# Optimization experiments

Measured on AMD Instinct MI355X. Metric: run time of the kernel, lower is better.

The kernel has to match this reference:

```python
import jax, jax.numpy as jnp
import numpy as np

N_NODES = 100000
N_EDGES = 400000
B = 1024
D_XD = 78
SEQ = 1000
EMB = 128
HID = 300
NF = 32
OUT_DIM = 128


def setup_inputs():
    key = jax.random.key(0)
    ks = jax.random.split(key, 40)
    rn = lambda k, s, sc=0.05: jax.random.normal(k, s, dtype=jnp.float32) * sc
    inp = {}
    inp['x'] = rn(ks[0], (N_NODES, D_XD), 1.0)
    inp['edge_index'] = jax.random.randint(ks[1], (2, N_EDGES), 0, N_NODES, dtype=jnp.int32)
    inp['batch'] = jnp.sort(jax.random.randint(ks[2], (N_NODES,), 0, B, dtype=jnp.int32))
    inp['target'] = jax.random.randint(ks[3], (B, SEQ), 0, 26, dtype=jnp.int32)
    inp['embs'] = rn(ks[4], (B * 13, 133), 1.0)
    inp['W1'] = rn(ks[5], (D_XD, D_XD)); inp['b1'] = jnp.zeros((D_XD,), jnp.float32)
    inp['W2'] = rn(ks[6], (D_XD, D_XD * 2)); inp['b2'] = jnp.zeros((D_XD * 2,), jnp.float32)
    inp['W3'] = rn(ks[7], (D_XD * 2, D_XD * 4)); inp['b3'] = jnp.zeros((D_XD * 4,), jnp.float32)
    inp['fc_g1_w'] = rn(ks[8], (D_XD * 4, 1024)); inp['fc_g1_b'] = jnp.zeros((1024,), jnp.float32)
    inp['fc_g2_w'] = rn(ks[9], (1024, OUT_DIM)); inp['fc_g2_b'] = jnp.zeros((OUT_DIM,), jnp.float32)
    inp['emb_xt'] = rn(ks[10], (26, EMB), 1.0)
    inp['conv_w'] = rn(ks[11], (NF, SEQ, 8)); inp['conv_b'] = jnp.zeros((NF,), jnp.float32)
    inp['fc1xt_w'] = rn(ks[12], (NF * 121, OUT_DIM)); inp['fc1xt_b'] = jnp.zeros((OUT_DIM,), jnp.float32)
    inp['fg_lin_w'] = rn(ks[13], (133, HID)); inp['fg_lin_b'] = jnp.zeros((HID,), jnp.float32)
    inp['Wq'] = rn(ks[14], (HID, HID)); inp['Wk'] = rn(ks[15], (HID, HID)); inp['Wv'] = rn(ks[16], (HID, HID))
    inp['ln_g'] = jnp.ones((HID,), jnp.float32); inp['ln_b'] = jnp.zeros((HID,), jnp.float32)
    inp['fg_out_w'] = rn(ks[17], (HID, OUT_DIM)); inp['fg_out_b'] = jnp.zeros((OUT_DIM,), jnp.float32)
    inp['fc1_w'] = rn(ks[18], (3 * OUT_DIM, 1024)); inp['fc1_b'] = jnp.zeros((1024,), jnp.float32)
    inp['fc2_w'] = rn(ks[19], (1024, 512)); inp['fc2_b'] = jnp.zeros((512,), jnp.float32)
    inp['out_w'] = rn(ks[20], (512, 1)); inp['out_b'] = jnp.zeros((1,), jnp.float32)
    return inp


def _gcn_conv(h_in, W, b, src, dst, dis):
    # PyG GCNConv: x' = D^-1/2 (A+I) D^-1/2 (X W) + b
    h = h_in @ W
    norm = dis[src] * dis[dst]  # [E]
    agg = jax.ops.segment_sum(h[src] * norm[:, None], dst, num_segments=h.shape[0])
    agg = agg + h * (dis * dis)[:, None]  # self-loop term
    return agg + b


def _forward(x, embs, W1, b1, W2, b2, W3, b3, fc_g1_w, fc_g1_b, fc_g2_w, fc_g2_b,
             emb_xt, conv_w, conv_b, fc1xt_w, fc1xt_b, fg_lin_w, fg_lin_b,
             Wq, Wk, Wv, ln_g, ln_b, fg_out_w, fg_out_b,
             fc1_w, fc1_b, fc2_w, fc2_b, out_w, out_b,
             edge_index, batch, target):
    src, dst = edge_index[0], edge_index[1]
    deg = jax.ops.segment_sum(jnp.ones_like(dst, jnp.float32), dst, num_segments=x.shape[0]) + 1.0
    dis = jax.lax.rsqrt(deg)
    h = jax.nn.relu(_gcn_conv(x, W1, b1, src, dst, dis))
    h = jax.nn.relu(_gcn_conv(h, W2, b2, src, dst, dis))
    h = jax.nn.relu(_gcn_conv(h, W3, b3, src, dst, dis))
    g = jax.ops.segment_max(h, batch, num_segments=B)  # global max pool
    g = jnp.where(jnp.isfinite(g), g, 0.0)
    g = jax.nn.relu(g @ fc_g1_w + fc_g1_b)
    g = g @ fc_g2_w + fc_g2_b  # dropout is identity at eval
    # protein branch: embedding + Conv1d(in=1000, out=32, k=8) over embed axis
    e = emb_xt[target]  # [B, SEQ, EMB]
    c = jax.lax.conv_general_dilated(e, conv_w, (1,), 'VALID',
                                     dimension_numbers=('NCH', 'OIH', 'NCH'))
    c = c + conv_b[None, :, None]  # [B, 32, 121]
    xt = c.reshape(B, NF * 121) @ fc1xt_w + fc1xt_b
    # functional-group prompt branch (KANO-style): linear -> self-attn -> LN -> gather row i*13
    f = (embs @ fg_lin_w + fg_lin_b).reshape(B, 13, HID)
    q = f @ Wq; k = f @ Wk; v = f @ Wv
    attn = jax.nn.softmax(jnp.einsum('bqd,bkd->bqk', q, k) / jnp.sqrt(jnp.float32(HID)), axis=-1)
    f2 = f + jnp.einsum('bqk,bkd->bqd', attn, v)
    mu = f2.mean(-1, keepdims=True)
    var = f2.var(-1, keepdims=True)
    f2 = (f2 - mu) * jax.lax.rsqrt(var + 1e-5) * ln_g + ln_b
    fg = f2[:, 0, :] @ fg_out_w + fg_out_b  # row i*13 per molecule
    xc = jnp.concatenate([g, xt, fg], axis=1)  # [B, 3*OUT_DIM]
    xc = jax.nn.relu(xc @ fc1_w + fc1_b)
    xc = jax.nn.relu(xc @ fc2_w + fc2_b)
    return xc @ out_w + out_b


def reference(x, edge_index, batch, target, embs, W1, b1, W2, b2, W3, b3,
              fc_g1_w, fc_g1_b, fc_g2_w, fc_g2_b, emb_xt, conv_w, conv_b,
              fc1xt_w, fc1xt_b, fg_lin_w, fg_lin_b, Wq, Wk, Wv, ln_g, ln_b,
              fg_out_w, fg_out_b, fc1_w, fc1_b, fc2_w, fc2_b, out_w, out_b):
    return _forward(x, embs, W1, b1, W2, b2, W3, b3, fc_g1_w, fc_g1_b, fc_g2_w, fc_g2_b,
                    emb_xt, conv_w, conv_b, fc1xt_w, fc1xt_b, fg_lin_w, fg_lin_b,
                    Wq, Wk, Wv, ln_g, ln_b, fg_out_w, fg_out_b,
                    fc1_w, fc1_b, fc2_w, fc2_b, out_w, out_b,
                    edge_index, batch, target)
```

## Files before the change

### kernel.cpp

```cpp
#include <hip/hip_runtime.h>
#include <hip/hip_bf16.h>
#include <math.h>

#define NNODES 100000
#define NEDGES 400000
#define NB     1024
#define SEQ    1000
#define HID    300
#define NBLK1  ((NNODES + 255) / 256)

typedef __attribute__((ext_vector_type(8))) short short8;
typedef __attribute__((ext_vector_type(4))) float f32x4;

__device__ __forceinline__ float bf_lo(unsigned int v) { return __uint_as_float(v << 16); }
__device__ __forceinline__ float bf_hi(unsigned int v) { return __uint_as_float(v & 0xffff0000u); }
__device__ __forceinline__ unsigned int bf_pack(float lo, float hi) {
    __hip_bfloat16 a = __float2bfloat16(lo), b = __float2bfloat16(hi);
    unsigned short ua = *(unsigned short*)&a, ub = *(unsigned short*)&b;
    return (unsigned int)ua | ((unsigned int)ub << 16);
}

__global__ void cvt_pad_kernel(const float* __restrict__ in, __hip_bfloat16* __restrict__ out,
                               int M, int K, int Kpad)
{
    long idx = (long)blockIdx.x * 256 + threadIdx.x;
    if (idx >= (long)M * Kpad) return;
    int m = idx / Kpad, k = idx % Kpad;
    out[idx] = __float2bfloat16(k < K ? in[(long)m * K + k] : 0.f);
}

__global__ void transpose_cvt_kernel(const float* __restrict__ in, __hip_bfloat16* __restrict__ out,
                                     int K, int N, int Kpad)
{
    long idx = (long)blockIdx.x * 256 + threadIdx.x;
    if (idx >= (long)N * Kpad) return;
    int n = idx / Kpad, k = idx % Kpad;
    out[idx] = __float2bfloat16(k < K ? in[(long)k * N + n] : 0.f);
}

struct TBatch {
    const float* src[12];
    __hip_bfloat16* dst[12];
    int K[12]; int N[12]; int Kpad[12];
    int bstart[13];
};

__global__ __launch_bounds__(256) void transpose_batch_kernel(TBatch tb)
{
    int blk = blockIdx.x;
    int d = 0;
    while (d < 11 && blk >= tb.bstart[d + 1]) ++d;
    long idx = (long)(blk - tb.bstart[d]) * 256 + threadIdx.x;
    long tot = (long)tb.N[d] * tb.Kpad[d];
    if (idx >= tot) return;
    int Kpad = tb.Kpad[d];
    int n = idx / Kpad, k = idx % Kpad;
    tb.dst[d][idx] = __float2bfloat16(k < tb.K[d] ? tb.src[d][(long)k * tb.N[d] + n] : 0.f);
}

__global__ __launch_bounds__(256) void gemm_bf16_kernel(
    const __hip_bfloat16* __restrict__ A, const __hip_bfloat16* __restrict__ Bt,
    const float* __restrict__ bias, void* __restrict__ C,
    int M, int N, int Kpad, int lda, int ldc, int Npad_out,
    int relu, int outbf, int chunk)
{
    __shared__ __align__(16) __hip_bfloat16 As[64][40];
    __shared__ __align__(16) __hip_bfloat16 Bs[64][40];
    int tid = threadIdx.x;
    int wave = tid >> 6, lane = tid & 63;
    int wm = wave >> 1, wn = wave & 1;
    int quad = lane >> 4, l16 = lane & 15;
    int row0 = blockIdx.y * 64, col0 = blockIdx.x * 64;

    int kbeg = 0, kend = Kpad;
    if (chunk > 0) { kbeg = blockIdx.z * chunk; kend = kbeg + chunk; if (kend > Kpad) kend = Kpad; }

    f32x4 acc[2][2];
    #pragma unroll
    for (int i = 0; i < 2; ++i)
        #pragma unroll
        for (int j = 0; j < 2; ++j) acc[i][j] = (f32x4){0.f, 0.f, 0.f, 0.f};

    int r = tid >> 2, cch = (tid & 3) * 8;

    for (int k0 = kbeg; k0 < kend; k0 += 32) {
        uint4 av = {0u, 0u, 0u, 0u};
        if (row0 + r < M) av = *(const uint4*)(A + (size_t)(row0 + r) * lda + k0 + cch);
        *(uint4*)(&As[r][cch]) = av;
        uint4 bv = {0u, 0u, 0u, 0u};
        if (col0 + r < N) bv = *(const uint4*)(Bt + (size_t)(col0 + r) * Kpad + k0 + cch);
        *(uint4*)(&Bs[r][cch]) = bv;
        __syncthreads();

        short8 a0 = *(const short8*)(&As[wm * 32 + l16][quad * 8]);
        short8 a1 = *(const short8*)(&As[wm * 32 + 16 + l16][quad * 8]);
        short8 b0 = *(const short8*)(&Bs[wn * 32 + l16][quad * 8]);
        short8 b1 = *(const short8*)(&Bs[wn * 32 + 16 + l16][quad * 8]);
        acc[0][0] = __builtin_amdgcn_mfma_f32_16x16x32_bf16(a0, b0, acc[0][0], 0, 0, 0);
        acc[0][1] = __builtin_amdgcn_mfma_f32_16x16x32_bf16(a0, b1, acc[0][1], 0, 0, 0);
        acc[1][0] = __builtin_amdgcn_mfma_f32_16x16x32_bf16(a1, b0, acc[1][0], 0, 0, 0);
        acc[1][1] = __builtin_amdgcn_mfma_f32_16x16x32_bf16(a1, b1, acc[1][1], 0, 0, 0);
        __syncthreads();
    }

    #pragma unroll
    for (int ti = 0; ti < 2; ++ti) {
        int rbase = row0 + wm * 32 + ti * 16 + quad * 4;
        #pragma unroll
        for (int tj = 0; tj < 2; ++tj) {
            int cc = col0 + wn * 32 + tj * 16 + l16;
            if (cc >= Npad_out) continue;
            #pragma unroll
            for (int reg = 0; reg < 4; ++reg) {
                int rr = rbase + reg;
                if (rr >= M) continue;
                float v = acc[ti][tj][reg];
                if (chunk > 0) {
                    if (cc < N) atomicAdd((float*)C + (size_t)rr * ldc + cc, v);
                } else {
                    float ov = 0.f;
                    if (cc < N) {
                        if (bias) v += bias[cc];
                        if (relu) v = fmaxf(v, 0.f);
                        ov = v;
                    }
                    if (outbf) ((__hip_bfloat16*)C)[(size_t)rr * ldc + cc] = __float2bfloat16(ov);
                    else       ((float*)C)[(size_t)rr * ldc + cc] = ov;
                }
            }
        }
    }
}

static void launch_gemm_bf16(const __hip_bfloat16* A, const __hip_bfloat16* Bt, const float* bias,
                             void* C, int M, int N, int Kpad, int lda, int ldc, int Npad_out,
                             int relu, int outbf, int splitz, hipStream_t stream)
{
    int cover = N > Npad_out ? N : Npad_out;
    int chunk = (splitz > 1) ? (Kpad / splitz) : 0;
    dim3 grid((cover + 63) / 64, (M + 63) / 64, splitz > 1 ? splitz : 1);
    gemm_bf16_kernel<<<grid, 256, 0, stream>>>(A, Bt, bias, C, M, N, Kpad, lda, ldc, Npad_out,
                                               relu, outbf, chunk);
}

__global__ void deg_kernel(const int* __restrict__ dst, int* __restrict__ deg, int E)
{
    int e = blockIdx.x * 256 + threadIdx.x;
    if (e < E) atomicAdd(&deg[dst[e]], 1);
}

__global__ void dis_kernel(const int* __restrict__ deg, float* __restrict__ dis,
                           float* __restrict__ selfc, int n)
{
    int i = blockIdx.x * 256 + threadIdx.x;
    if (i < n) {
        float d = (float)deg[i] + 1.0f;
        float r = 1.0f / sqrtf(d);
        dis[i] = r;
        selfc[i] = r * r;
    }
}

__global__ __launch_bounds__(256) void scan_p1(const int* __restrict__ deg,
                                               int* __restrict__ off, int* __restrict__ bsum)
{
    __shared__ int s[256];
    int tid = threadIdx.x;
    int i = blockIdx.x * 256 + tid;
    int v = (i < NNODES) ? deg[i] : 0;
    s[tid] = v;
    __syncthreads();
    #pragma unroll
    for (int d = 1; d < 256; d <<= 1) {
        int t = (tid >= d) ? s[tid - d] : 0;
        __syncthreads();
        s[tid] += t;
        __syncthreads();
    }
    if (i < NNODES) off[i] = s[tid] - v;
    if (tid == 255) bsum[blockIdx.x] = s[255];
}

__global__ __launch_bounds__(512) void scan_p2(int* __restrict__ bsum)
{
    __shared__ int s[512];
    int tid = threadIdx.x;
    int v = (tid < NBLK1) ? bsum[tid] : 0;
    s[tid] = v;
    __syncthreads();
    #pragma unroll
    for (int d = 1; d < 512; d <<= 1) {
        int t = (tid >= d) ? s[tid - d] : 0;
        __syncthreads();
        s[tid] += t;
        __syncthreads();
    }
    if (tid < NBLK1) bsum[tid] = s[tid] - v;
}

__global__ __launch_bounds__(256) void scan_p3(int* __restrict__ off, const int* __restrict__ bsum,
                                               int* __restrict__ cur)
{
    int i = blockIdx.x * 256 + threadIdx.x;
    if (i < NNODES) {
        int v = off[i] + bsum[blockIdx.x];
        off[i] = v;
        cur[i] = v;
    }
    if (i == NNODES) off[NNODES] = NEDGES;
}

__global__ void fill_csr_kernel(const int* __restrict__ src, const int* __restrict__ dst,
                                const float* __restrict__ dis, int* __restrict__ cur,
                                int* __restrict__ csr_src, float* __restrict__ csr_w, int E)
{
    int e = blockIdx.x * 256 + threadIdx.x;
    if (e >= E) return;
    int s = src[e], d = dst[e];
    int p = atomicAdd(&cur[d], 1);
    csr_src[p] = s;
    csr_w[p] = dis[s] * dis[d];
}

__global__ __launch_bounds__(256) void gcn_agg2(
    const __hip_bfloat16* __restrict__ Tin, const int* __restrict__ off,
    const int* __restrict__ csr_src, const float* __restrict__ csr_w,
    const float* __restrict__ selfc, __hip_bfloat16* __restrict__ out,
    int half, int nc)
{
    int wave = threadIdx.x >> 6, lane = threadIdx.x & 63;
    int node = blockIdx.x * 4 + wave;
    if (node >= NNODES) return;
    const unsigned int* Tp = (const unsigned int*)Tin;
    unsigned int* Op = (unsigned int*)out;
    size_t rb = (size_t)node * half;
    bool m0 = lane < half;
    bool m1 = (nc > 1) && (lane + 64 < half);
    float sc = selfc[node];
    float a0x = 0.f, a0y = 0.f, a1x = 0.f, a1y = 0.f;
    if (m0) { unsigned int v = Tp[rb + lane];      a0x = bf_lo(v) * sc; a0y = bf_hi(v) * sc; }
    if (m1) { unsigned int v = Tp[rb + lane + 64]; a1x = bf_lo(v) * sc; a1y = bf_hi(v) * sc; }
    int s0 = off[node], s1 = off[node + 1];
    for (int e = s0; e < s1; ++e) {
        size_t sb = (size_t)csr_src[e] * half;
        float w = csr_w[e];
        if (m0) { unsigned int v = Tp[sb + lane];      a0x += bf_lo(v) * w; a0y += bf_hi(v) * w; }
        if (m1) { unsigned int v = Tp[sb + lane + 64]; a1x += bf_lo(v) * w; a1y += bf_hi(v) * w; }
    }
    if (m0) Op[rb + lane]      = bf_pack(a0x, a0y);
    if (m1) Op[rb + lane + 64] = bf_pack(a1x, a1y);
}

__global__ __launch_bounds__(256) void pool_max_bf16(
    const __hip_bfloat16* __restrict__ H, const int* __restrict__ batch,
    __hip_bfloat16* __restrict__ g)
{
    int b = blockIdx.x;
    int lo = 0, hi = NNODES;
    while (lo < hi) { int mid = (lo + hi) >> 1; if (batch[mid] < b) lo = mid + 1; else hi = mid; }
    int s = lo;
    hi = NNODES;
    while (lo < hi) { int mid = (lo + hi) >> 1; if (batch[mid] < b + 1) lo = mid + 1; else hi = mid; }
    int e = lo;
    int tid = threadIdx.x;
    if (tid < 160) {
        const unsigned int* Hp = (const unsigned int*)H;
        float mx = 0.f, my = 0.f;
        for (int i = s; i < e; ++i) {
            unsigned int v = Hp[(size_t)i * 160 + tid];
            mx = fmaxf(mx, bf_lo(v));
            my = fmaxf(my, bf_hi(v));
        }
        ((unsigned int*)g)[(size_t)b * 160 + tid] = bf_pack(mx, my);
    }
}

__global__ void conv_transpose_kernel(const float* __restrict__ w, float* __restrict__ wt)
{
    int idx = blockIdx.x * 256 + threadIdx.x;
    if (idx >= 256000) return;
    int o = idx / 8000;
    int rem = idx - o * 8000;
    int i = rem >> 3, k = rem & 7;
    wt[i * 256 + o * 8 + k] = w[idx];
}

__global__ __launch_bounds__(256) void conv_agg_kernel(
    const float* __restrict__ cwt, const int* __restrict__ target,
    __hip_bfloat16* __restrict__ aggw)
{
    int b = blockIdx.x, tid = threadIdx.x;
    __shared__ float s[26 * 256];
    for (int i = tid; i < 26 * 256; i += 256) s[i] = 0.f;
    __syncthreads();
    const int* tb = target + b * SEQ;
    for (int i = 0; i < SEQ; ++i) {
        int a = tb[i];
        s[a * 256 + tid] += cwt[i * 256 + tid];
    }
    __syncthreads();
    for (int i = tid; i < 26 * 256; i += 256)
        aggw[(size_t)b * 6656 + i] = __float2bfloat16(s[i]);
}

__global__ __launch_bounds__(128) void conv_wc_kernel(
    const float* __restrict__ emb, const float* __restrict__ w_fc, float* __restrict__ Wc)
{
    int o = blockIdx.x;
    int ak = blockIdx.y;
    int a = ak >> 3, k = ak & 7;
    int j = threadIdx.x;
    const float* wp = w_fc + (long)(o * 121) * 128 + j;
    const float* ep = emb + a * 128 + k;
    float s = 0.f;
    #pragma unroll 11
    for (int t = 0; t < 121; ++t) s += ep[t] * wp[t * 128];
    Wc[(long)(a * 256 + o * 8 + k) * 128 + j] = s;
}

__global__ void xtb_init_kernel(const float* __restrict__ b_fc, float* __restrict__ xtb)
{
    xtb[threadIdx.x] = b_fc[threadIdx.x];
}

__global__ __launch_bounds__(128) void convb_fold_kernel(
    const float* __restrict__ w_fc, const float* __restrict__ conv_b, float* __restrict__ xtb)
{
    int o = blockIdx.x, j = threadIdx.x;
    const float* wp = w_fc + (long)(o * 121) * 128 + j;
    float s = 0.f;
    for (int t = 0; t < 121; ++t) s += wp[t * 128];
    atomicAdd(&xtb[j], s * conv_b[o]);
}

__global__ void xc_convbias_kernel(const float* __restrict__ xtb, float* __restrict__ xc)
{
    int idx = blockIdx.x * 256 + threadIdx.x;
    if (idx >= NB * 128) return;
    int b = idx >> 7, j = idx & 127;
    xc[(long)b * 384 + 128 + j] = xtb[j];
}

__global__ __launch_bounds__(256) void attn_ln_kernel(
    const __hip_bfloat16* __restrict__ Fb, const __hip_bfloat16* __restrict__ Kf,
    const __hip_bfloat16* __restrict__ Vf, const __hip_bfloat16* __restrict__ q0,
    const float* __restrict__ ln_g, const float* __restrict__ ln_b,
    __hip_bfloat16* __restrict__ out)
{
    int b = blockIdx.x, tid = threadIdx.x;
    __shared__ float qs[HID];
    __shared__ float sc[13];
    __shared__ float red[256];
    __shared__ float red2[256];
    __shared__ float rowv[HID];
    __shared__ float mean_s, inv_s;

    for (int d = tid; d < HID; d += 256) qs[d] = __bfloat162float(q0[(size_t)b * 320 + d]);
    __syncthreads();
    if (tid < 208) {
        int k = tid >> 4, sub = tid & 15;
        const __hip_bfloat16* kr = Kf + ((size_t)b * 13 + k) * 320;
        float p = 0.f;
        for (int d = sub; d < HID; d += 16) p += qs[d] * __bfloat162float(kr[d]);
        red[tid] = p;
    }
    __syncthreads();
    if (tid < 208 && (tid & 15) == 0) {
        float s = 0.f;
        #pragma unroll
        for (int j = 0; j < 16; ++j) s += red[tid + j];
        sc[tid >> 4] = s * 0.0577350269189626f;
    }
    __syncthreads();
    if (tid == 0) {
        float mx = sc[0];
        for (int k = 1; k < 13; ++k) mx = fmaxf(mx, sc[k]);
        float ssum = 0.f;
        for (int k = 0; k < 13; ++k) { float e = expf(sc[k] - mx); sc[k] = e; ssum += e; }
        float inv = 1.0f / ssum;
        for (int k = 0; k < 13; ++k) sc[k] *= inv;
    }
    __syncthreads();
    for (int d = tid; d < HID; d += 256) {
        float v = __bfloat162float(Fb[((size_t)b * 13) * 320 + d]);
        #pragma unroll
        for (int k = 0; k < 13; ++k)
            v += sc[k] * __bfloat162float(Vf[((size_t)b * 13 + k) * 320 + d]);
        rowv[d] = v;
    }
    __syncthreads();
    float s1 = 0.f, s2 = 0.f;
    for (int d = tid; d < HID; d += 256) { float v = rowv[d]; s1 += v; s2 += v * v; }
    red[tid] = s1; red2[tid] = s2;
    __syncthreads();
    for (int s = 128; s > 0; s >>= 1) {
        if (tid < s) { red[tid] += red[tid + s]; red2[tid] += red2[tid + s]; }
        __syncthreads();
    }
    if (tid == 0) {
        float mean = red[0] / (float)HID;
        float var = red2[0] / (float)HID - mean * mean;
        mean_s = mean;
        inv_s = 1.0f / sqrtf(var + 1e-5f);
    }
    __syncthreads();
    for (int d = tid; d < 320; d += 256) {
        float v = 0.f;
        if (d < HID) v = (rowv[d] - mean_s) * inv_s * ln_g[d] + ln_b[d];
        out[(size_t)b * 320 + d] = __float2bfloat16(v);
    }
}

__global__ __launch_bounds__(256) void final_out_kernel(
    const float* __restrict__ X, const float* __restrict__ w,
    const float* __restrict__ bias, float* __restrict__ out)
{
    int b = blockIdx.x, tid = threadIdx.x;
    __shared__ float red[256];
    float p = X[(long)b * 512 + tid] * w[tid] + X[(long)b * 512 + tid + 256] * w[tid + 256];
    red[tid] = p;
    __syncthreads();
    for (int s = 128; s > 0; s >>= 1) {
        if (tid < s) red[tid] += red[tid + s];
        __syncthreads();
    }
    if (tid == 0) out[b] = red[0] + bias[0];
}

extern "C" void kernel_launch(void* const* d_in, const int* in_sizes, int n_in,
                              void* d_out, int out_size, void* d_ws, size_t ws_size,
                              hipStream_t stream)
{
    const float* x        = (const float*)d_in[0];
    const int*   ei       = (const int*)d_in[1];
    const int*   batch    = (const int*)d_in[2];
    const int*   target   = (const int*)d_in[3];
    const float* embs     = (const float*)d_in[4];
    const float* W1       = (const float*)d_in[5];
    const float* b1       = (const float*)d_in[6];
    const float* W2       = (const float*)d_in[7];
    const float* b2       = (const float*)d_in[8];
    const float* W3       = (const float*)d_in[9];
    const float* b3       = (const float*)d_in[10];
    const float* fc_g1_w  = (const float*)d_in[11];
    const float* fc_g1_b  = (const float*)d_in[12];
    const float* fc_g2_w  = (const float*)d_in[13];
    const float* fc_g2_b  = (const float*)d_in[14];
    const float* emb_xt   = (const float*)d_in[15];
    const float* conv_w   = (const float*)d_in[16];
    const float* conv_b   = (const float*)d_in[17];
    const float* fc1xt_w  = (const float*)d_in[18];
    const float* fc1xt_b  = (const float*)d_in[19];
    const float* fg_lin_w = (const float*)d_in[20];
    const float* fg_lin_b = (const float*)d_in[21];
    const float* Wq       = (const float*)d_in[22];
    const float* Wk       = (const float*)d_in[23];
    const float* Wv       = (const float*)d_in[24];
    const float* ln_g     = (const float*)d_in[25];
    const float* ln_b     = (const float*)d_in[26];
    const float* fg_out_w = (const float*)d_in[27];
    const float* fg_out_b = (const float*)d_in[28];
    const float* fc1_w    = (const float*)d_in[29];
    const float* fc1_b    = (const float*)d_in[30];
    const float* fc2_w    = (const float*)d_in[31];
    const float* fc2_b    = (const float*)d_in[32];
    const float* out_w    = (const float*)d_in[33];
    const float* out_b    = (const float*)d_in[34];

    const int* src = ei;
    const int* dst = ei + NEDGES;
    typedef __hip_bfloat16 bf;

    char* p = (char*)d_ws;
    auto alloc = [&](size_t bytes) { char* r = p; p += (bytes + 255) & ~(size_t)255; return r; };
    bf*   xb      = (bf*)alloc((size_t)NNODES * 96 * 2);
    bf*   T       = (bf*)alloc((size_t)NNODES * 160 * 2);
    bf*   H       = (bf*)alloc((size_t)NNODES * 320 * 2);
    int*  deg     = (int*)alloc(NNODES * 4);
    float* dis    = (float*)alloc(NNODES * 4);
    float* selfc  = (float*)alloc(NNODES * 4);
    int*  off     = (int*)alloc((NNODES + 1) * 4);
    int*  bsum    = (int*)alloc(512 * 4);
    int*  csr_src = (int*)alloc(NEDGES * 4);
    float* csr_w  = (float*)alloc(NEDGES * 4);
    bf*   w1t     = (bf*)alloc(78 * 96 * 2);
    bf*   w2t     = (bf*)alloc(156 * 96 * 2);
    bf*   w3t     = (bf*)alloc(312 * 160 * 2);
    bf*   fcg1t   = (bf*)alloc(1024 * 320 * 2);
    bf*   fcg2t   = (bf*)alloc(128 * 1024 * 2);
    bf*   fglint  = (bf*)alloc(300 * 160 * 2);
    bf*   wkt     = (bf*)alloc(300 * 320 * 2);
    bf*   wvt     = (bf*)alloc(300 * 320 * 2);
    bf*   wqt     = (bf*)alloc(300 * 320 * 2);
    bf*   fgoutt  = (bf*)alloc(128 * 320 * 2);
    bf*   fc1t    = (bf*)alloc(1024 * 384 * 2);
    bf*   fc2t    = (bf*)alloc(512 * 1024 * 2);
    bf*   g       = (bf*)alloc((size_t)NB * 320 * 2);
    bf*   G1b     = (bf*)alloc((size_t)NB * 1024 * 2);
    bf*   embsb   = (bf*)alloc((size_t)NB * 13 * 160 * 2);
    bf*   Fbuf    = (bf*)alloc((size_t)NB * 13 * 320 * 2);
    bf*   Kbuf    = (bf*)alloc((size_t)NB * 13 * 320 * 2);
    bf*   Vbuf    = (bf*)alloc((size_t)NB * 13 * 320 * 2);
    bf*   Qbuf    = (bf*)alloc((size_t)NB * 320 * 2);
    bf*   f2row   = (bf*)alloc((size_t)NB * 320 * 2);
    float* xc     = (float*)alloc((size_t)NB * 384 * 4);
    bf*   xcb     = (bf*)alloc((size_t)NB * 384 * 2);
    float* F2     = (float*)alloc((size_t)NB * 512 * 4);
    float* cwt    = (float*)alloc(256000 * 4);
    bf*   aggwb   = (bf*)alloc((size_t)NB * 6656 * 2);
    float* Wc     = (float*)alloc((size_t)6656 * 128 * 4);
    bf*   Wct     = (bf*)alloc((size_t)128 * 6656 * 2);
    float* xtb    = (float*)alloc(128 * 4);

    hipMemsetAsync(deg, 0, NNODES * sizeof(int), stream);
    deg_kernel<<<(NEDGES + 255) / 256, 256, 0, stream>>>(dst, deg, NEDGES);
    dis_kernel<<<(NNODES + 255) / 256, 256, 0, stream>>>(deg, dis, selfc, NNODES);
    scan_p1<<<NBLK1, 256, 0, stream>>>(deg, off, bsum);
    scan_p2<<<1, 512, 0, stream>>>(bsum);
    scan_p3<<<NBLK1, 256, 0, stream>>>(off, bsum, deg);
    fill_csr_kernel<<<(NEDGES + 255) / 256, 256, 0, stream>>>(src, dst, dis, deg, csr_src, csr_w, NEDGES);

    {
        TBatch tb;
        const float* srcs[12] = {W1, W2, W3, fc_g1_w, fc_g2_w, fg_lin_w, Wk, Wv, Wq, fg_out_w, fc1_w, fc2_w};
        bf* dsts[12]          = {w1t, w2t, w3t, fcg1t, fcg2t, fglint, wkt, wvt, wqt, fgoutt, fc1t, fc2t};
        int Ks[12]    = {78, 78, 156, 312, 1024, 133, 300, 300, 300, 300, 384, 1024};
        int Ns[12]    = {78, 156, 312, 1024, 128, 300, 300, 300, 300, 128, 1024, 512};
        int Kpads[12] = {96, 96, 160, 320, 1024, 160, 320, 320, 320, 320, 384, 1024};
        int bs = 0;
        for (int i = 0; i < 12; ++i) {
            tb.src[i] = srcs[i]; tb.dst[i] = dsts[i];
            tb.K[i] = Ks[i]; tb.N[i] = Ns[i]; tb.Kpad[i] = Kpads[i];
            tb.bstart[i] = bs;
            bs += (int)(((long)Ns[i] * Kpads[i] + 255) / 256);
        }
        tb.bstart[12] = bs;
        transpose_batch_kernel<<<bs, 256, 0, stream>>>(tb);
    }
    cvt_pad_kernel<<<((long)NNODES * 96 + 255) / 256, 256, 0, stream>>>(x, xb, NNODES, 78, 96);
    cvt_pad_kernel<<<((long)NB * 13 * 160 + 255) / 256, 256, 0, stream>>>(embs, embsb, NB * 13, 133, 160);

    int agrid = (NNODES + 3) / 4;
    gcn_agg2<<<agrid, 256, 0, stream>>>(xb, off, csr_src, csr_w, selfc, T, 48, 1);
    launch_gemm_bf16(T, w1t, b1, H, NNODES, 78, 96, 96, 96, 96, 1, 1, 1, stream);

    gcn_agg2<<<agrid, 256, 0, stream>>>(H, off, csr_src, csr_w, selfc, T, 48, 1);
    launch_gemm_bf16(T, w2t, b2, H, NNODES, 156, 96, 96, 160, 160, 1, 1, 1, stream);

    gcn_agg2<<<agrid, 256, 0, stream>>>(H, off, csr_src, csr_w, selfc, T, 80, 2);
    launch_gemm_bf16(T, w3t, b3, H, NNODES, 312, 160, 160, 320, 320, 1, 1, 1, stream);

    pool_max_bf16<<<NB, 256, 0, stream>>>(H, batch, g);
    launch_gemm_bf16(g, fcg1t, fc_g1_b, G1b, NB, 1024, 320, 320, 1024, 1024, 1, 1, 1, stream);
    launch_gemm_bf16(G1b, fcg2t, fc_g2_b, xc, NB, 128, 1024, 1024, 384, 128, 0, 0, 1, stream);

    conv_transpose_kernel<<<(256000 + 255) / 256, 256, 0, stream>>>(conv_w, cwt);
    conv_agg_kernel<<<NB, 256, 0, stream>>>(cwt, target, aggwb);
    conv_wc_kernel<<<dim3(32, 208), 128, 0, stream>>>(emb_xt, fc1xt_w, Wc);
    transpose_cvt_kernel<<<((long)128 * 6656 + 255) / 256, 256, 0, stream>>>(Wc, Wct, 6656, 128, 6656);
    xtb_init_kernel<<<1, 128, 0, stream>>>(fc1xt_b, xtb);
    convb_fold_kernel<<<32, 128, 0, stream>>>(fc1xt_w, conv_b, xtb);
    xc_convbias_kernel<<<(NB * 128 + 255) / 256, 256, 0, stream>>>(xtb, xc);
    launch_gemm_bf16(aggwb, Wct, nullptr, xc + 128, NB, 128, 6656, 6656, 384, 128, 0, 0, 8, stream);

    launch_gemm_bf16(embsb, fglint, fg_lin_b, Fbuf, NB * 13, 300, 160, 160, 320, 320, 0, 1, 1, stream);
    launch_gemm_bf16(Fbuf, wkt, nullptr, Kbuf, NB * 13, 300, 320, 320, 320, 320, 0, 1, 1, stream);
    launch_gemm_bf16(Fbuf, wvt, nullptr, Vbuf, NB * 13, 300, 320, 320, 320, 320, 0, 1, 1, stream);
    launch_gemm_bf16(Fbuf, wqt, nullptr, Qbuf, NB, 300, 320, 13 * 320, 320, 320, 0, 1, 1, stream);
    attn_ln_kernel<<<NB, 256, 0, stream>>>(Fbuf, Kbuf, Vbuf, Qbuf, ln_g, ln_b, f2row);
    launch_gemm_bf16(f2row, fgoutt, fg_out_b, xc + 256, NB, 128, 320, 320, 384, 128, 0, 0, 1, stream);

    cvt_pad_kernel<<<((long)NB * 384 + 255) / 256, 256, 0, stream>>>(xc, xcb, NB, 384, 384);
    launch_gemm_bf16(xcb, fc1t, fc1_b, G1b, NB, 1024, 384, 384, 1024, 1024, 1, 1, 1, stream);
    launch_gemm_bf16(G1b, fc2t, fc2_b, F2, NB, 512, 1024, 1024, 512, 512, 1, 0, 1, stream);
    final_out_kernel<<<NB, 256, 0, stream>>>(F2, out_w, out_b, (float*)d_out);
}
```

Before: 841.2 us.

## Bucket conv aggregation by token, store conv weights in bf16, unroll GCN gather

The conv aggregation kernel now loads each sequence's tokens into shared memory, counting-sorts positions into 26 buckets, and sums transposed conv weights per bucket in registers. This replaces the read-modify-write loop on a large shared accumulator. The transposed conv weights are stored as bf16 to halve their read traffic, which adds a rounding step before summation. The GCN aggregation loop is unrolled by two with separate accumulators so two neighbour rows are loaded in flight at once. The bucketing adds serial per-thread scans over the sequence done by only 26 threads.

```diff
diff --git a/kernel.cpp b/kernel.cpp
--- a/kernel.cpp
+++ b/kernel.cpp
@@ -238,17 +238,36 @@
     bool m1 = (nc > 1) && (lane + 64 < half);
     float sc = selfc[node];
     float a0x = 0.f, a0y = 0.f, a1x = 0.f, a1y = 0.f;
+    float b0x = 0.f, b0y = 0.f, b1x = 0.f, b1y = 0.f;
     if (m0) { unsigned int v = Tp[rb + lane];      a0x = bf_lo(v) * sc; a0y = bf_hi(v) * sc; }
     if (m1) { unsigned int v = Tp[rb + lane + 64]; a1x = bf_lo(v) * sc; a1y = bf_hi(v) * sc; }
     int s0 = off[node], s1 = off[node + 1];
-    for (int e = s0; e < s1; ++e) {
-        size_t sb = (size_t)csr_src[e] * half;
-        float w = csr_w[e];
-        if (m0) { unsigned int v = Tp[sb + lane];      a0x += bf_lo(v) * w; a0y += bf_hi(v) * w; }
-        if (m1) { unsigned int v = Tp[sb + lane + 64]; a1x += bf_lo(v) * w; a1y += bf_hi(v) * w; }
-    }
-    if (m0) Op[rb + lane]      = bf_pack(a0x, a0y);
-    if (m1) Op[rb + lane + 64] = bf_pack(a1x, a1y);
+    int e = s0;
+    for (; e + 2 <= s1; e += 2) {
+        int i0 = csr_src[e], i1 = csr_src[e + 1];
+        float w0 = csr_w[e], w1 = csr_w[e + 1];
+        size_t p0 = (size_t)i0 * half, p1 = (size_t)i1 * half;
+        unsigned int v00 = 0u, v01 = 0u, v10 = 0u, v11 = 0u;
+        if (m0) { v00 = Tp[p0 + lane]; v10 = Tp[p1 + lane]; }
+        if (m1) { v01 = Tp[p0 + lane + 64]; v11 = Tp[p1 + lane + 64]; }
+        if (m0) {
+            a0x += bf_lo(v00) * w0; a0y += bf_hi(v00) * w0;
+            b0x += bf_lo(v10) * w1; b0y += bf_hi(v10) * w1;
+        }
+        if (m1) {
+            a1x += bf_lo(v01) * w0; a1y += bf_hi(v01) * w0;
+            b1x += bf_lo(v11) * w1; b1y += bf_hi(v11) * w1;
+        }
+    }
+    if (e < s1) {
+        int i0 = csr_src[e];
+        float w0 = csr_w[e];
+        size_t p0 = (size_t)i0 * half;
+        if (m0) { unsigned int v = Tp[p0 + lane];      a0x += bf_lo(v) * w0; a0y += bf_hi(v) * w0; }
+        if (m1) { unsigned int v = Tp[p0 + lane + 64]; a1x += bf_lo(v) * w0; a1y += bf_hi(v) * w0; }
+    }
+    if (m0) Op[rb + lane]      = bf_pack(a0x + b0x, a0y + b0y);
+    if (m1) Op[rb + lane + 64] = bf_pack(a1x + b1x, a1y + b1y);
 }
 
 __global__ __launch_bounds__(256) void pool_max_bf16(
@@ -275,32 +294,55 @@
     }
 }
 
-__global__ void conv_transpose_kernel(const float* __restrict__ w, float* __restrict__ wt)
+__global__ void conv_transpose_kernel(const float* __restrict__ w, __hip_bfloat16* __restrict__ wt)
 {
     int idx = blockIdx.x * 256 + threadIdx.x;
     if (idx >= 256000) return;
     int o = idx / 8000;
     int rem = idx - o * 8000;
     int i = rem >> 3, k = rem & 7;
-    wt[i * 256 + o * 8 + k] = w[idx];
+    wt[i * 256 + o * 8 + k] = __float2bfloat16(w[idx]);
 }
 
 __global__ __launch_bounds__(256) void conv_agg_kernel(
-    const float* __restrict__ cwt, const int* __restrict__ target,
+    const __hip_bfloat16* __restrict__ cwt, const int* __restrict__ target,
     __hip_bfloat16* __restrict__ aggw)
 {
+    __shared__ int tb_s[SEQ];
+    __shared__ int boff[27];
+    __shared__ int bucket[SEQ];
     int b = blockIdx.x, tid = threadIdx.x;
-    __shared__ float s[26 * 256];
-    for (int i = tid; i < 26 * 256; i += 256) s[i] = 0.f;
-    __syncthreads();
     const int* tb = target + b * SEQ;
-    for (int i = 0; i < SEQ; ++i) {
-        int a = tb[i];
-        s[a * 256 + tid] += cwt[i * 256 + tid];
-    }
-    __syncthreads();
-    for (int i = tid; i < 26 * 256; i += 256)
-        aggw[(size_t)b * 6656 + i] = __float2bfloat16(s[i]);
+    for (int i = tid; i < SEQ; i += 256) tb_s[i] = tb[i];
+    __syncthreads();
+    if (tid < 26) {
+        int c = 0;
+        for (int i = 0; i < SEQ; ++i) c += (tb_s[i] == tid);
+        boff[tid + 1] = c;
+    }
+    __syncthreads();
+    if (tid == 0) {
+        boff[0] = 0;
+        for (int a = 1; a <= 26; ++a) boff[a] += boff[a - 1];
+    }
+    __syncthreads();
+    if (tid < 26) {
+        int w = boff[tid];
+        for (int i = 0; i < SEQ; ++i)
+            if (tb_s[i] == tid) bucket[w++] = i;
+    }
+    __syncthreads();
+    for (int a = 0; a < 26; ++a) {
+        int s = boff[a], e = boff[a + 1];
+        float acc0 = 0.f, acc1 = 0.f;
+        int j = s;
+        for (; j + 2 <= e; j += 2) {
+            acc0 += __bfloat162float(cwt[bucket[j] * 256 + tid]);
+            acc1 += __bfloat162float(cwt[bucket[j + 1] * 256 + tid]);
+        }
+        if (j < e) acc0 += __bfloat162float(cwt[bucket[j] * 256 + tid]);
+        aggw[(size_t)b * 6656 + a * 256 + tid] = __float2bfloat16(acc0 + acc1);
+    }
 }
 
 __global__ __launch_bounds__(128) void conv_wc_kernel(
@@ -506,7 +548,7 @@
     float* xc     = (float*)alloc((size_t)NB * 384 * 4);
     bf*   xcb     = (bf*)alloc((size_t)NB * 384 * 2);
     float* F2     = (float*)alloc((size_t)NB * 512 * 4);
-    float* cwt    = (float*)alloc(256000 * 4);
+    bf*   cwt     = (bf*)alloc(256000 * 2);
     bf*   aggwb   = (bf*)alloc((size_t)NB * 6656 * 2);
     float* Wc     = (float*)alloc((size_t)6656 * 128 * 4);
     bf*   Wct     = (bf*)alloc((size_t)128 * 6656 * 2);
```

Result: slower. 862.4 us (+2.5%).
